# Kernel optimization log

Hardware: AMD Instinct MI355X
Metric: run time of the kernel (lower is better)

## Reference

```python
import math
import jax, jax.numpy as jnp
import numpy as np
from jax import lax

TAU_P = 0.5  # forward arg tau_p, fixed

def _grid_boxes(H, W, g):
    boxes = []
    for r in range(g):
        for c in range(g):
            x0 = int(round(c * (W / float(g)))); y0 = int(round(r * (H / float(g))))
            x1 = int(round((c + 1) * (W / float(g)))) - 1; y1 = int(round((r + 1) * (H / float(g)))) - 1
            boxes.append((x0, y0, x1, y1))
    return boxes

def _box_masks(H, W, g):
    bs = _grid_boxes(H, W, g)
    m = np.zeros((len(bs), H, W), np.float32)
    for i, (x0, y0, x1, y1) in enumerate(bs):
        m[i, y0:y1 + 1, x0:x1 + 1] = 1.0
    return jnp.asarray(m)

def _ln(x, g, b, eps=1e-5):
    mu = x.mean(-1, keepdims=True)
    v = jnp.var(x, axis=-1, keepdims=True)
    return (x - mu) * lax.rsqrt(v + eps) * g + b

def _l2n(x):
    return x / jnp.maximum(jnp.linalg.norm(x, axis=-1, keepdims=True), 1e-12)

def _forward(x, conv1_w, proj_w, proj_b, ln1_g, ln1_b, Wqkv, bqkv, Wo, bo,
             ln2_g, ln2_b, W1, b1, W2, b2, tln_g, tln_b, slot_q, cls_w, cls_b,
             use_spmask, spmask_grid):
    d = slot_q.shape[1]; M = slot_q.shape[0]; nhead = 4; dh = d // nhead
    # conv1 (1->150, k9 s2 p4) + exact gelu + 1x1 proj to d_model
    h = lax.conv_general_dilated(x, conv1_w, (2, 2), [(4, 4), (4, 4)],
                                 dimension_numbers=('NCHW', 'OIHW', 'NCHW'))
    h = jax.nn.gelu(h, approximate=False)
    h = jnp.einsum('bchw,dc->bdhw', h, proj_w) + proj_b[None, :, None, None]
    B, _, H, W = h.shape
    tokens = h.transpose(0, 2, 3, 1).reshape(B, H * W, d)  # (B,N,d)
    # pre-norm transformer encoder layer (1 layer)
    t1 = _ln(tokens, ln1_g, ln1_b)
    qkv = t1 @ Wqkv.T + bqkv
    q, k, v = jnp.split(qkv, 3, axis=-1)
    sh = lambda a: a.reshape(B, -1, nhead, dh).transpose(0, 2, 1, 3)
    q, k, v = sh(q), sh(k), sh(v)
    attn = jax.nn.softmax(jnp.einsum('bhnd,bhmd->bhnm', q, k) / math.sqrt(dh), axis=-1)
    o = jnp.einsum('bhnm,bhmd->bhnd', attn, v).transpose(0, 2, 1, 3).reshape(B, -1, d)
    tokens = tokens + o @ Wo.T + bo
    t2 = _ln(tokens, ln2_g, ln2_b)
    tokens = tokens + jax.nn.gelu(t2 @ W1.T + b1, approximate=False) @ W2.T + b2
    tokens = _ln(tokens, tln_g, tln_b)
    # slot attention logits, softmax over tokens
    A_logits = jnp.einsum('md,bnd->bmn', _l2n(slot_q), _l2n(tokens)) / math.sqrt(d)
    A_slot = jax.nn.softmax(A_logits, axis=2).reshape(B, M, H, W)
    if use_spmask:
        bm = _box_masks(H, W, spmask_grid)               # (G,H,W) static 0/1 masks
        mass = jnp.einsum('bmhw,ghw->bmg', A_slot, bm)   # per-cell mass
        _, top2 = lax.top_k(mass, 2)                     # (B,M,2) top-2 cells
        umask = jnp.maximum(bm[top2[..., 0]], bm[top2[..., 1]])  # union mask (B,M,H,W)
        A_eff = A_slot * umask
        s = jnp.maximum(A_eff.reshape(B, M, -1).sum(-1), 1e-8)
        A_eff = A_eff / s[:, :, None, None]
        m2 = A_eff.reshape(B, M, -1).sum(-1)             # post-renorm mass (torch order)
        z = (m2 - m2.mean(axis=1, keepdims=True)) / TAU_P
    else:
        A_eff = A_slot
        lse = jax.nn.logsumexp(A_logits, axis=2)
        z = (lse - lse.mean(axis=1, keepdims=True)) / TAU_P
    P = jax.nn.softmax(z, axis=1)                        # (B,M)
    S = jnp.einsum('bmn,bnd->bmd', A_eff.reshape(B, M, H * W), tokens)
    S = _l2n(S)
    slot_logits = S @ cls_w.T + cls_b                    # (B,M,C)
    return (slot_logits * P[..., None]).sum(axis=1)      # (B,C)

def setup_inputs() -> dict:
    key = jax.random.key(0)
    ks = jax.random.split(key, 16)
    d, M, C, dff = 64, 12, 47, 256
    n = lambda k, shape, s=0.05: (jax.random.normal(k, shape, dtype=jnp.float32) * s)
    return {
        'x': jax.random.normal(ks[0], (2048, 1, 28, 28), dtype=jnp.float32),
        'conv1_w': n(ks[1], (150, 1, 9, 9), 0.1),
        'proj_w': n(ks[2], (d, 150), 0.1), 'proj_b': jnp.zeros((d,), jnp.float32),
        'ln1_g': jnp.ones((d,), jnp.float32), 'ln1_b': jnp.zeros((d,), jnp.float32),
        'Wqkv': n(ks[3], (3 * d, d), 0.1), 'bqkv': jnp.zeros((3 * d,), jnp.float32),
        'Wo': n(ks[4], (d, d), 0.1), 'bo': jnp.zeros((d,), jnp.float32),
        'ln2_g': jnp.ones((d,), jnp.float32), 'ln2_b': jnp.zeros((d,), jnp.float32),
        'W1': n(ks[5], (dff, d), 0.1), 'b1': jnp.zeros((dff,), jnp.float32),
        'W2': n(ks[6], (d, dff), 0.1), 'b2': jnp.zeros((d,), jnp.float32),
        'tln_g': jnp.ones((d,), jnp.float32), 'tln_b': jnp.zeros((d,), jnp.float32),
        'slot_q': n(ks[7], (M, d), 1.0 / math.sqrt(d)),
        'cls_w': n(ks[8], (C, d), 0.1), 'cls_b': jnp.zeros((C,), jnp.float32),
        'use_spmask': 1, 'spmask_grid': 2,
    }

def reference(x, conv1_w, proj_w, proj_b, ln1_g, ln1_b, Wqkv, bqkv, Wo, bo,
              ln2_g, ln2_b, W1, b1, W2, b2, tln_g, tln_b, slot_q, cls_w, cls_b,
              use_spmask, spmask_grid):
    return _forward(x, conv1_w, proj_w, proj_b, ln1_g, ln1_b, Wqkv, bqkv, Wo, bo,
                    ln2_g, ln2_b, W1, b1, W2, b2, tln_g, tln_b, slot_q, cls_w, cls_b,
                    use_spmask, spmask_grid)
```

## Files before the change

### kernel.cpp

```cpp
#include <hip/hip_runtime.h>
#include <math.h>

typedef _Float16 half_t;
typedef __attribute__((ext_vector_type(2))) _Float16 half2t;
typedef __attribute__((ext_vector_type(4))) _Float16 half4;
typedef __attribute__((ext_vector_type(8))) _Float16 half8;
typedef __attribute__((ext_vector_type(4))) float f32x4;

__device__ __forceinline__ f32x4 MFMA16(half4 a, half4 b, f32x4 c) {
  return __builtin_amdgcn_mfma_f32_16x16x16f16(a, b, c, 0, 0, 0);
}
__device__ __forceinline__ f32x4 MFMA32(half8 a, half8 b, f32x4 c) {
  return __builtin_amdgcn_mfma_f32_16x16x32_f16(a, b, c, 0, 0, 0);
}

#if __has_builtin(__builtin_amdgcn_exp2f)
#define EXP2F(x) __builtin_amdgcn_exp2f(x)
#else
#define EXP2F(x) exp2f(x)
#endif

__device__ __forceinline__ half2t cvt_pk(float a, float b) {
#if __has_builtin(__builtin_amdgcn_cvt_pkrtz)
  return __builtin_bit_cast(half2t, __builtin_amdgcn_cvt_pkrtz(a, b));
#else
  half2t r; r[0] = (half_t)a; r[1] = (half_t)b; return r;
#endif
}
__device__ __forceinline__ half4 PK4(float a, float b, float c, float d) {
  half2t lo = cvt_pk(a, b), hi = cvt_pk(c, d);
  return __builtin_shufflevector(lo, hi, 0, 1, 2, 3);
}

__device__ __forceinline__ int SWi(int row, int col) {
  return (row << 6) | (((((col >> 2) ^ row) & 15)) << 2) | (col & 3);
}
__device__ __forceinline__ int SW4i(int row, int q) {
  return (row << 6) | ((((q ^ row) & 15)) << 2);
}
__device__ __forceinline__ int XH8W(int t, int k0) {
  return (t << 6) | ((((k0 >> 3) ^ t) & 7) << 3) | (k0 & 7);
}
__device__ __forceinline__ int XH8R(int t, int u8) {
  return (t << 6) | (((u8 ^ t) & 7) << 3);
}

__device__ __forceinline__ float fast_gelu(float v) {
  float x = 0.70710678118654752f * v;
  float ax = fabsf(x);
  float t = 1.0f / fmaf(0.3275911f, ax, 1.0f);
  float poly = t * fmaf(t, fmaf(t, fmaf(t, fmaf(t, 1.061405429f, -1.453152027f),
                                        1.421413741f), -0.284496736f), 0.254829592f);
  float e = EXP2F(-1.4426950408889634f * ax * ax);
  float erfax = fmaf(-poly, e, 1.0f);
  float er = __builtin_copysignf(erfax, x);
  return 0.5f * v * (1.0f + er);
}

__global__ void k_prepack(const float* __restrict__ conv_w,
                          const float* __restrict__ proj_w,
                          const float* __restrict__ Wqkv,
                          const float* __restrict__ Wo,
                          const float* __restrict__ W1,
                          const float* __restrict__ W2,
                          half_t* __restrict__ dst) {
  int id = blockIdx.x * 512 + threadIdx.x;
  if (id < 7552) {
    int unit = id >> 6, ln = id & 63;
    int li = ln & 15, g8 = (ln >> 4) * 8;
    float v[8];
    if (unit < 24) {
      int rt = unit >> 1, ks2 = unit & 1;
      const float* s = &Wqkv[(rt * 16 + li) * 64 + ks2 * 32 + g8];
#pragma unroll
      for (int r = 0; r < 8; ++r) v[r] = s[r];
    } else if (unit < 56) {
      int u = unit - 24, rt = u >> 1, ks2 = u & 1;
      const float* s = &W1[(rt * 16 + li) * 64 + ks2 * 32 + g8];
#pragma unroll
      for (int r = 0; r < 8; ++r) v[r] = s[r];
    } else if (unit < 88) {
      int u = unit - 56, ct = u >> 3, ks2 = u & 7;
      const float* s = &W2[(ct * 16 + li) * 256 + ks2 * 32 + g8];
#pragma unroll
      for (int r = 0; r < 8; ++r) v[r] = s[r];
    } else {
      int u = unit - 88, ct = u / 3, ks2 = u - ct * 3;
      int row = ct * 16 + li;
#pragma unroll
      for (int r = 0; r < 8; ++r) {
        int col = ks2 * 32 + g8 + r;
        v[r] = (row < 150 && col < 81) ? conv_w[row * 81 + col] : 0.f;
      }
    }
    half8 o;
#pragma unroll
    for (int r = 0; r < 8; ++r) o[r] = (half_t)v[r];
    ((half8*)dst)[id] = o;
  } else if (id < 11136) {
    int id2 = id - 7552;
    int unit = id2 >> 6, ln = id2 & 63;
    int li = ln & 15, gq = (ln >> 4) * 4;
    float v[4];
    if (unit < 16) {
      int ct = unit >> 2, h = unit & 3;
      const float* s = &Wo[(ct * 16 + li) * 64 + h * 16 + gq];
#pragma unroll
      for (int r = 0; r < 4; ++r) v[r] = s[r];
    } else {
      int u = unit - 16, dt = u / 10, ct = u - dt * 10;
#pragma unroll
      for (int r = 0; r < 4; ++r) {
        int col = ct * 16 + gq + r;
        v[r] = (col < 150) ? proj_w[(dt * 16 + li) * 150 + col] : 0.f;
      }
    }
    half4 o;
#pragma unroll
    for (int r = 0; r < 4; ++r) o[r] = (half_t)v[r];
    ((half4*)(dst + 60416))[id2] = o;
  }
}

__global__ __launch_bounds__(512, 4) void k_net(
    const float* __restrict__ x,
    const half8* __restrict__ WQ8, const half8* __restrict__ W18,
    const half8* __restrict__ W28, const half8* __restrict__ Wc8,
    const half4* __restrict__ WO4, const half4* __restrict__ Pw4,
    const float* __restrict__ proj_b,
    const float* __restrict__ ln1_g, const float* __restrict__ ln1_b,
    const float* __restrict__ bqkv, const float* __restrict__ bo,
    const float* __restrict__ ln2_g, const float* __restrict__ ln2_b,
    const float* __restrict__ b1, const float* __restrict__ b2,
    const float* __restrict__ tln_g, const float* __restrict__ tln_b,
    float* __restrict__ tokens) {
  extern __shared__ __align__(16) char pool[];
  half_t* xsh = (half_t*)pool;
  half_t* Xh = (half_t*)pool;
  half_t* Kb = (half_t*)(pool + 26624);
  half_t* VT = (half_t*)(pool + 43264);
  half8* W1S = (half8*)(pool + 26624);
  half8* W2S = (half8*)(pool + 34816);
  half_t* Hb = (half_t*)(pool + 43008);
  float* OS = (float*)pool;

  const int b = blockIdx.x, tid = threadIdx.x;
  const int wv = tid >> 6, ln = tid & 63, g = ln >> 4, li = ln & 15;
  const size_t base = (size_t)b * 12544;
  const half_t h1 = (half_t)1.f;
  const half4 ones = {h1, h1, h1, h1};

  f32x4 res[2][4];
#pragma unroll
  for (int qi = 0; qi < 2; ++qi)
#pragma unroll
    for (int ct = 0; ct < 4; ++ct) res[qi][ct] = f32x4{0.f, 0.f, 0.f, 0.f};

  for (int i = tid; i < 1260; i += 512) xsh[i] = (half_t)0.f;
  __syncthreads();
  for (int i = tid; i < 784; i += 512) {
    int r = i / 28, c = i - r * 28;
    xsh[(r + 4) * 36 + c + 4] = (half_t)x[b * 784 + i];
  }
  __syncthreads();

#pragma unroll
  for (int qi = 0; qi < 2; ++qi) {
    int qt = wv + 8 * qi;
    if (qt < 13) {
      int pp = qt * 16 + li;
      int pc = (pp < 196) ? pp : 195;
      int oy = pc / 14, ox = pc - oy * 14;
      int pbase = oy * 72 + ox * 2;
      half8 bf[3];
#pragma unroll
      for (int ks2 = 0; ks2 < 3; ++ks2) {
#pragma unroll
        for (int j = 0; j < 8; ++j) {
          int tap = ks2 * 32 + g * 8 + j;
          half_t v = (half_t)0.f;
          if (tap <= 80) {
            int ky = tap / 9;
            v = xsh[pbase + ky * 27 + tap];
          }
          bf[ks2][j] = v;
        }
      }
#pragma unroll
      for (int ct = 0; ct < 10; ++ct) {
        f32x4 acc = {0.f, 0.f, 0.f, 0.f};
#pragma unroll
        for (int ks2 = 0; ks2 < 3; ++ks2)
          acc = MFMA32(Wc8[(ct * 3 + ks2) * 64 + ln], bf[ks2], acc);
        half4 hf = PK4(fast_gelu(acc[0]), fast_gelu(acc[1]),
                       fast_gelu(acc[2]), fast_gelu(acc[3]));
#pragma unroll
        for (int dt = 0; dt < 4; ++dt)
          res[qi][dt] = MFMA16(Pw4[(dt * 10 + ct) * 64 + ln], hf, res[qi][dt]);
      }
#pragma unroll
      for (int dt = 0; dt < 4; ++dt) {
        float4 pb4 = *(const float4*)&proj_b[dt * 16 + g * 4];
        res[qi][dt][0] += pb4.x; res[qi][dt][1] += pb4.y;
        res[qi][dt][2] += pb4.z; res[qi][dt][3] += pb4.w;
      }
    }
  }
  __syncthreads();

  for (int i = tid; i < 768; i += 512)
    Xh[(196 + (i >> 6)) * 64 + (i & 63)] = (half_t)0.f;
#pragma unroll
  for (int qi = 0; qi < 2; ++qi) {
    int qt = wv + 8 * qi;
    if (qt < 13) {
      float sum = 0.f;
#pragma unroll
      for (int ct = 0; ct < 4; ++ct)
#pragma unroll
        for (int r = 0; r < 4; ++r) sum += res[qi][ct][r];
      sum += __shfl_xor(sum, 16, 64);
      sum += __shfl_xor(sum, 32, 64);
      float mu = sum * 0.015625f;
      float vs = 0.f;
#pragma unroll
      for (int ct = 0; ct < 4; ++ct)
#pragma unroll
        for (int r = 0; r < 4; ++r) { float d = res[qi][ct][r] - mu; vs += d * d; }
      vs += __shfl_xor(vs, 16, 64);
      vs += __shfl_xor(vs, 32, 64);
      float rs = rsqrtf(vs * 0.015625f + 1e-5f);
      int t = qt * 16 + li;
      if (t < 196) {
#pragma unroll
        for (int ct = 0; ct < 4; ++ct) {
          int k0 = ct * 16 + g * 4;
          float4 gg = *(const float4*)&ln1_g[k0];
          float4 bb = *(const float4*)&ln1_b[k0];
          *(half4*)&Xh[XH8W(t, k0)] =
              PK4((res[qi][ct][0] - mu) * rs * gg.x + bb.x,
                  (res[qi][ct][1] - mu) * rs * gg.y + bb.y,
                  (res[qi][ct][2] - mu) * rs * gg.z + bb.z,
                  (res[qi][ct][3] - mu) * rs * gg.w + bb.w);
        }
      }
    }
  }
  __syncthreads();

  half4 qf[2][4];
#pragma unroll
  for (int qi = 0; qi < 2; ++qi) {
    int qt = wv + 8 * qi;
    if (qt < 13) {
#pragma unroll
      for (int h = 0; h < 4; ++h) {
        f32x4 acc = {0.f, 0.f, 0.f, 0.f};
#pragma unroll
        for (int ks2 = 0; ks2 < 2; ++ks2)
          acc = MFMA32(WQ8[(h * 2 + ks2) * 64 + ln],
                       *(const half8*)&Xh[XH8R(qt * 16 + li, ks2 * 4 + g)], acc);
        const float SC = 0.36067376022224085f;
        qf[qi][h] = PK4((acc[0] + bqkv[h * 16 + g * 4 + 0]) * SC,
                        (acc[1] + bqkv[h * 16 + g * 4 + 1]) * SC,
                        (acc[2] + bqkv[h * 16 + g * 4 + 2]) * SC,
                        (acc[3] + bqkv[h * 16 + g * 4 + 3]) * SC);
      }
    }
  }

  for (int p = 0; p < 2; ++p) {
    {
      int rt4 = wv & 3, hh = rt4 & 1;
      bool isK = rt4 < 2;
      int rtg = (isK ? 4 : 8) + 2 * p + hh;
      half8 af[2];
#pragma unroll
      for (int ks2 = 0; ks2 < 2; ++ks2) af[ks2] = WQ8[(rtg * 2 + ks2) * 64 + ln];
      float bias[4];
      int brow = (isK ? 64 : 128) + (2 * p + hh) * 16 + g * 4;
#pragma unroll
      for (int r = 0; r < 4; ++r) bias[r] = bqkv[brow + r];
      int ta = (wv < 4) ? 0 : 7, tz = (wv < 4) ? 7 : 13;
      for (int tt = ta; tt < tz; ++tt) {
        int trow = tt * 16 + li;
        f32x4 acc = {0.f, 0.f, 0.f, 0.f};
#pragma unroll
        for (int ks2 = 0; ks2 < 2; ++ks2)
          acc = MFMA32(af[ks2], *(const half8*)&Xh[XH8R(trow, ks2 * 4 + g)], acc);
        if (isK) {
          *(half4*)&Kb[(hh * 208 + trow) * 20 + g * 4] =
              PK4(acc[0] + bias[0], acc[1] + bias[1],
                  acc[2] + bias[2], acc[3] + bias[3]);
        } else {
#pragma unroll
          for (int r = 0; r < 4; ++r)
            VT[(hh * 16 + g * 4 + r) * 212 + trow] = (half_t)(acc[r] + bias[r]);
        }
      }
    }
    __syncthreads();
#pragma unroll
    for (int qi = 0; qi < 2; ++qi) {
      int qt = wv + 8 * qi;
      if (qt < 13) {
#pragma unroll
        for (int hh = 0; hh < 2; ++hh) {
          int hglob = 2 * p + hh;
          f32x4 oa = {0.f, 0.f, 0.f, 0.f};
          f32x4 o1 = {0.f, 0.f, 0.f, 0.f};
#pragma unroll
          for (int nt = 0; nt < 13; ++nt) {
            f32x4 zz = {0.f, 0.f, 0.f, 0.f};
            f32x4 sv = MFMA16(*(const half4*)&Kb[(hh * 208 + nt * 16 + li) * 20 + g * 4],
                              qf[qi][hglob], zz);
            if (nt == 12 && g > 0) { sv[0] = -3e38f; sv[1] = -3e38f; sv[2] = -3e38f; sv[3] = -3e38f; }
            half4 pf = PK4(EXP2F(sv[0]), EXP2F(sv[1]), EXP2F(sv[2]), EXP2F(sv[3]));
            oa = MFMA16(*(const half4*)&VT[(hh * 16 + li) * 212 + nt * 16 + g * 4],
                        pf, oa);
            o1 = MFMA16(ones, pf, o1);
          }
          float inv = 1.0f / o1[0];
          half4 of = PK4(oa[0] * inv, oa[1] * inv, oa[2] * inv, oa[3] * inv);
#pragma unroll
          for (int ct = 0; ct < 4; ++ct)
            res[qi][ct] = MFMA16(WO4[(ct * 4 + hglob) * 64 + ln], of, res[qi][ct]);
        }
      }
    }
    __syncthreads();
  }
#pragma unroll
  for (int qi = 0; qi < 2; ++qi) {
    int qt = wv + 8 * qi;
    if (qt < 13) {
#pragma unroll
      for (int ct = 0; ct < 4; ++ct) {
        float4 bb = *(const float4*)&bo[ct * 16 + g * 4];
        res[qi][ct][0] += bb.x; res[qi][ct][1] += bb.y;
        res[qi][ct][2] += bb.z; res[qi][ct][3] += bb.w;
      }
    }
  }

#pragma unroll
  for (int qi = 0; qi < 2; ++qi) {
    int qt = wv + 8 * qi;
    if (qt < 13) {
      float sum = 0.f;
#pragma unroll
      for (int ct = 0; ct < 4; ++ct)
#pragma unroll
        for (int r = 0; r < 4; ++r) sum += res[qi][ct][r];
      sum += __shfl_xor(sum, 16, 64);
      sum += __shfl_xor(sum, 32, 64);
      float mu = sum * 0.015625f;
      float vs = 0.f;
#pragma unroll
      for (int ct = 0; ct < 4; ++ct)
#pragma unroll
        for (int r = 0; r < 4; ++r) { float d = res[qi][ct][r] - mu; vs += d * d; }
      vs += __shfl_xor(vs, 16, 64);
      vs += __shfl_xor(vs, 32, 64);
      float rs = rsqrtf(vs * 0.015625f + 1e-5f);
      int t = qt * 16 + li;
      if (t < 196) {
#pragma unroll
        for (int ct = 0; ct < 4; ++ct) {
          int k0 = ct * 16 + g * 4;
          float4 gg = *(const float4*)&ln2_g[k0];
          float4 bb = *(const float4*)&ln2_b[k0];
          *(half4*)&Xh[XH8W(t, k0)] =
              PK4((res[qi][ct][0] - mu) * rs * gg.x + bb.x,
                  (res[qi][ct][1] - mu) * rs * gg.y + bb.y,
                  (res[qi][ct][2] - mu) * rs * gg.z + bb.z,
                  (res[qi][ct][3] - mu) * rs * gg.w + bb.w);
        }
      }
    }
  }
  __syncthreads();

  for (int ch = 0; ch < 4; ++ch) {
    {
      int u = tid >> 6, l2 = tid & 63;
      int lnt = u >> 1, ks2 = u & 1;
      W1S[u * 64 + l2] = W18[((ch * 4 + lnt) * 2 + ks2) * 64 + l2];
      int ct = u >> 1, k2 = u & 1;
      W2S[u * 64 + l2] = W28[(ct * 8 + ch * 2 + k2) * 64 + l2];
    }
    __syncthreads();
#pragma unroll
    for (int j = 0; j < 7; ++j) {
      int u = wv + 8 * j;
      if (u < 52) {
        int mt = u >> 2, lnt = u & 3;
        f32x4 acc = {0.f, 0.f, 0.f, 0.f};
#pragma unroll
        for (int ks2 = 0; ks2 < 2; ++ks2)
          acc = MFMA32(*(const half8*)&Xh[XH8R(mt * 16 + li, ks2 * 4 + g)],
                       W1S[(lnt * 2 + ks2) * 64 + ln], acc);
        float bb = b1[ch * 64 + lnt * 16 + li];
#pragma unroll
        for (int r = 0; r < 4; ++r)
          Hb[XH8W(mt * 16 + g * 4 + r, lnt * 16 + li)] = (half_t)fast_gelu(acc[r] + bb);
      }
    }
    __syncthreads();
#pragma unroll
    for (int qi = 0; qi < 2; ++qi) {
      int qt = wv + 8 * qi;
      if (qt < 13) {
#pragma unroll
        for (int ct = 0; ct < 4; ++ct)
#pragma unroll
          for (int k2 = 0; k2 < 2; ++k2)
            res[qi][ct] = MFMA32(W2S[(ct * 2 + k2) * 64 + ln],
                                 *(const half8*)&Hb[XH8R(qt * 16 + li, k2 * 4 + g)],
                                 res[qi][ct]);
      }
    }
    __syncthreads();
  }
#pragma unroll
  for (int qi = 0; qi < 2; ++qi) {
    int qt = wv + 8 * qi;
    if (qt < 13) {
#pragma unroll
      for (int ct = 0; ct < 4; ++ct) {
        float4 bb = *(const float4*)&b2[ct * 16 + g * 4];
        res[qi][ct][0] += bb.x; res[qi][ct][1] += bb.y;
        res[qi][ct][2] += bb.z; res[qi][ct][3] += bb.w;
      }
    }
  }

#pragma unroll
  for (int qi = 0; qi < 2; ++qi) {
    int qt = wv + 8 * qi;
    if (qt < 13) {
      float sum = 0.f;
#pragma unroll
      for (int ct = 0; ct < 4; ++ct)
#pragma unroll
        for (int r = 0; r < 4; ++r) sum += res[qi][ct][r];
      sum += __shfl_xor(sum, 16, 64);
      sum += __shfl_xor(sum, 32, 64);
      float mu = sum * 0.015625f;
      float vs = 0.f;
#pragma unroll
      for (int ct = 0; ct < 4; ++ct)
#pragma unroll
        for (int r = 0; r < 4; ++r) { float d = res[qi][ct][r] - mu; vs += d * d; }
      vs += __shfl_xor(vs, 16, 64);
      vs += __shfl_xor(vs, 32, 64);
      float rs = rsqrtf(vs * 0.015625f + 1e-5f);
#pragma unroll
      for (int ct = 0; ct < 4; ++ct) {
        float4 gg = *(const float4*)&tln_g[ct * 16 + g * 4];
        float4 bb = *(const float4*)&tln_b[ct * 16 + g * 4];
        float4 o;
        o.x = (res[qi][ct][0] - mu) * rs * gg.x + bb.x;
        o.y = (res[qi][ct][1] - mu) * rs * gg.y + bb.y;
        o.z = (res[qi][ct][2] - mu) * rs * gg.z + bb.z;
        o.w = (res[qi][ct][3] - mu) * rs * gg.w + bb.w;
        *(float4*)&OS[wv * 1088 + li * 68 + ct * 16 + g * 4] = o;
      }
#pragma unroll
      for (int rep = 0; rep < 4; ++rep) {
        int r4 = rep * 64 + ln;
        int row = r4 >> 4, q = r4 & 15;
        int pp = qt * 16 + row;
        if (pp < 196)
          *(float4*)&tokens[base + (size_t)pp * 64 + q * 4] =
              *(const float4*)&OS[wv * 1088 + row * 68 + q * 4];
      }
    }
  }
}

__global__ __launch_bounds__(256) void k_slots(
    const float* __restrict__ tokens, const float* __restrict__ slot_q,
    const float* __restrict__ cls_w, const float* __restrict__ cls_b,
    const int* __restrict__ use_spmask_p, const int* __restrict__ grid_p,
    float* __restrict__ out) {
  __shared__ float TOK[12544];
  __shared__ float Abuf[12 * 196];
  __shared__ float SQS[12 * 64];
  __shared__ float INV[196];
  __shared__ float VV[64];
  __shared__ float Pv[12];
  __shared__ float M2[12];
  __shared__ float ISN[12];
  __shared__ float ZS[2];

  const int b = blockIdx.x, tid = threadIdx.x;
  const size_t base = (size_t)b * 12544;
  (void)grid_p;

  for (int i = tid; i < 12544; i += 256) {
    int t = i >> 6, c = i & 63;
    TOK[SWi(t, c)] = tokens[base + i];
  }
  __syncthreads();
  if (tid < 196) {
    float ss = 0.f;
#pragma unroll
    for (int q = 0; q < 16; ++q) {
      float4 v = *(const float4*)&TOK[SW4i(tid, q)];
      ss += v.x * v.x + v.y * v.y + v.z * v.z + v.w * v.w;
    }
    INV[tid] = 1.0f / fmaxf(sqrtf(ss), 1e-12f);
  }
  if (tid < 192) {
    int m = tid >> 4, l = tid & 15;
    float ss = 0.f;
#pragma unroll
    for (int c = l; c < 64; c += 16) {
      float v = slot_q[m * 64 + c];
      ss += v * v;
    }
#pragma unroll
    for (int mm = 8; mm; mm >>= 1) ss += __shfl_xor(ss, mm, 64);
    float invq = 1.0f / fmaxf(sqrtf(ss), 1e-12f);
#pragma unroll
    for (int c = l; c < 64; c += 16) SQS[m * 64 + c] = slot_q[m * 64 + c] * invq;
  }
  __syncthreads();
  for (int i = tid; i < 2352; i += 256) {
    int m = i / 196, n = i - m * 196;
    float d = 0.f;
#pragma unroll
    for (int q = 0; q < 16; ++q) {
      float4 tv = *(const float4*)&TOK[SW4i(n, q)];
      float4 sv = *(const float4*)&SQS[m * 64 + q * 4];
      d += tv.x * sv.x + tv.y * sv.y + tv.z * sv.z + tv.w * sv.w;
    }
    Abuf[i] = d * INV[n] * 0.125f;
  }
  __syncthreads();
  const int use_spmask = *use_spmask_p;
  if (tid < 192) {
    int m = tid >> 4, l = tid & 15;
    float* Am = Abuf + m * 196;
    float mx = -1e30f;
    for (int n = l; n < 196; n += 16) mx = fmaxf(mx, Am[n]);
#pragma unroll
    for (int mm = 8; mm; mm >>= 1) mx = fmaxf(mx, __shfl_xor(mx, mm, 64));
    float se = 0.f, mc0 = 0.f, mc1 = 0.f, mc2 = 0.f, mc3 = 0.f;
    for (int n = l; n < 196; n += 16) {
      float e = __expf(Am[n] - mx);
      Am[n] = e;
      se += e;
      int yy = n / 14, xx = n - yy * 14;
      int cell = ((yy >= 7) ? 2 : 0) + ((xx >= 7) ? 1 : 0);
      mc0 += (cell == 0) ? e : 0.f;
      mc1 += (cell == 1) ? e : 0.f;
      mc2 += (cell == 2) ? e : 0.f;
      mc3 += (cell == 3) ? e : 0.f;
    }
#pragma unroll
    for (int mm = 8; mm; mm >>= 1) {
      se += __shfl_xor(se, mm, 64);
      mc0 += __shfl_xor(mc0, mm, 64);
      mc1 += __shfl_xor(mc1, mm, 64);
      mc2 += __shfl_xor(mc2, mm, 64);
      mc3 += __shfl_xor(mc3, mm, 64);
    }
    float invse = 1.0f / se;
    if (use_spmask) {
      int g1 = 0; float bv1 = mc0;
      if (mc1 > bv1) { bv1 = mc1; g1 = 1; }
      if (mc2 > bv1) { bv1 = mc2; g1 = 2; }
      if (mc3 > bv1) { bv1 = mc3; g1 = 3; }
      int g2 = -1; float bv2 = -1e30f;
      if (g1 != 0 && mc0 > bv2) { bv2 = mc0; g2 = 0; }
      if (g1 != 1 && mc1 > bv2) { bv2 = mc1; g2 = 1; }
      if (g1 != 2 && mc2 > bv2) { bv2 = mc2; g2 = 2; }
      if (g1 != 3 && mc3 > bv2) { bv2 = mc3; g2 = 3; }
      float sacc = 0.f;
      for (int n = l; n < 196; n += 16) {
        float a = Am[n] * invse;
        Am[n] = a;
        int yy = n / 14, xx = n - yy * 14;
        int cell = ((yy >= 7) ? 2 : 0) + ((xx >= 7) ? 1 : 0);
        sacc += (cell == g1 || cell == g2) ? a : 0.f;
      }
#pragma unroll
      for (int mm = 8; mm; mm >>= 1) sacc += __shfl_xor(sacc, mm, 64);
      float invs = 1.0f / fmaxf(sacc, 1e-8f);
      float m2acc = 0.f;
      for (int n = l; n < 196; n += 16) {
        int yy = n / 14, xx = n - yy * 14;
        int cell = ((yy >= 7) ? 2 : 0) + ((xx >= 7) ? 1 : 0);
        float a = (cell == g1 || cell == g2) ? (Am[n] * invs) : 0.f;
        Am[n] = a;
        m2acc += a;
      }
#pragma unroll
      for (int mm = 8; mm; mm >>= 1) m2acc += __shfl_xor(m2acc, mm, 64);
      if (l == 0) M2[m] = m2acc;
    } else {
      for (int n = l; n < 196; n += 16) Am[n] *= invse;
      if (l == 0) M2[m] = mx + logf(se);
    }
  }
  __syncthreads();
  if (tid == 0) {
    float mean = 0.f;
    for (int m = 0; m < 12; ++m) mean += M2[m];
    mean *= (1.0f / 12.0f);
    float zmax = -1e30f;
    for (int m = 0; m < 12; ++m) {
      float z = (M2[m] - mean) * 2.0f;
      Pv[m] = z;
      zmax = fmaxf(zmax, z);
    }
    float seP = 0.f;
    for (int m = 0; m < 12; ++m) {
      float e = __expf(Pv[m] - zmax);
      Pv[m] = e;
      seP += e;
    }
    float invP = 1.0f / seP;
    float sump = 0.f;
    for (int m = 0; m < 12; ++m) {
      float p = Pv[m] * invP;
      Pv[m] = p;
      sump += p;
    }
    ZS[0] = sump;
  }
  __syncthreads();
  for (int i = tid; i < 768; i += 256) {
    int m = i >> 6, c = i & 63;
    float a2 = 0.f;
    const float* Am = Abuf + m * 196;
    for (int n = 0; n < 196; ++n) a2 += Am[n] * TOK[SWi(n, c)];
    SQS[m * 64 + c] = a2;
  }
  __syncthreads();
  if (tid < 192) {
    int m = tid >> 4, l = tid & 15;
    float ss = 0.f;
#pragma unroll
    for (int c = l; c < 64; c += 16) {
      float v = SQS[m * 64 + c];
      ss += v * v;
    }
#pragma unroll
    for (int mm = 8; mm; mm >>= 1) ss += __shfl_xor(ss, mm, 64);
    if (l == 0) ISN[m] = 1.0f / fmaxf(sqrtf(ss), 1e-12f);
  }
  __syncthreads();
  if (tid < 64) {
    float v = 0.f;
#pragma unroll
    for (int m = 0; m < 12; ++m) v += Pv[m] * ISN[m] * SQS[m * 64 + tid];
    VV[tid] = v;
  }
  __syncthreads();
  if (tid < 47) {
    float a2 = 0.f;
#pragma unroll
    for (int q = 0; q < 16; ++q) {
      float4 w = *(const float4*)&cls_w[tid * 64 + q * 4];
      float4 v = *(const float4*)&VV[q * 4];
      a2 += w.x * v.x + w.y * v.y + w.z * v.z + w.w * v.w;
    }
    out[(size_t)b * 47 + tid] = a2 + cls_b[tid] * ZS[0];
  }
}

extern "C" void kernel_launch(void* const* d_in, const int* in_sizes, int n_in,
                              void* d_out, int out_size, void* d_ws, size_t ws_size,
                              hipStream_t stream) {
  (void)n_in; (void)out_size; (void)ws_size;
  const float* x      = (const float*)d_in[0];
  const float* conv_w = (const float*)d_in[1];
  const float* proj_w = (const float*)d_in[2];
  const float* proj_b = (const float*)d_in[3];
  const float* ln1_g  = (const float*)d_in[4];
  const float* ln1_b  = (const float*)d_in[5];
  const float* Wqkv   = (const float*)d_in[6];
  const float* bqkv   = (const float*)d_in[7];
  const float* Wo     = (const float*)d_in[8];
  const float* bo     = (const float*)d_in[9];
  const float* ln2_g  = (const float*)d_in[10];
  const float* ln2_b  = (const float*)d_in[11];
  const float* W1     = (const float*)d_in[12];
  const float* b1     = (const float*)d_in[13];
  const float* W2     = (const float*)d_in[14];
  const float* b2     = (const float*)d_in[15];
  const float* tln_g  = (const float*)d_in[16];
  const float* tln_b  = (const float*)d_in[17];
  const float* slot_q = (const float*)d_in[18];
  const float* cls_w  = (const float*)d_in[19];
  const float* cls_b  = (const float*)d_in[20];
  const int* use_spm  = (const int*)d_in[21];
  const int* spgrid   = (const int*)d_in[22];

  const int B = in_sizes[0] / 784;
  half_t* wsh = (half_t*)d_ws;
  const half8* WQ8 = (const half8*)wsh;
  const half8* W18 = (const half8*)(wsh + 12288);
  const half8* W28 = (const half8*)(wsh + 28672);
  const half8* Wc8 = (const half8*)(wsh + 45056);
  const half4* WO4 = (const half4*)(wsh + 60416);
  const half4* Pw4 = (const half4*)(wsh + 64512);
  float* tokens = (float*)((char*)d_ws + 163840);

  k_prepack<<<22, 512, 0, stream>>>(conv_w, proj_w, Wqkv, Wo, W1, W2, wsh);

  const int shnet = 69632;
  (void)hipFuncSetAttribute((const void*)k_net,
                            hipFuncAttributeMaxDynamicSharedMemorySize, shnet);
  k_net<<<B, 512, shnet, stream>>>(x, WQ8, W18, W28, Wc8, WO4, Pw4, proj_b,
                                   ln1_g, ln1_b, bqkv, bo, ln2_g, ln2_b,
                                   b1, b2, tln_g, tln_b, tokens);

  k_slots<<<B, 256, 0, stream>>>(tokens, slot_q, cls_w, cls_b, use_spm, spgrid,
                                 (float*)d_out);
}
```

Baseline: 399.8 us.

## Fuse slot-attention kernel into transformer kernel, keeping tokens in LDS

```diff
diff --git a/kernel.cpp b/kernel.cpp
--- a/kernel.cpp
+++ b/kernel.cpp
@@ -133,7 +133,9 @@
     const float* __restrict__ ln2_g, const float* __restrict__ ln2_b,
     const float* __restrict__ b1, const float* __restrict__ b2,
     const float* __restrict__ tln_g, const float* __restrict__ tln_b,
-    float* __restrict__ tokens) {
+    const float* __restrict__ slot_q, const float* __restrict__ cls_w,
+    const float* __restrict__ cls_b, const int* __restrict__ use_spmask_p,
+    float* __restrict__ out) {
   extern __shared__ __align__(16) char pool[];
   half_t* xsh = (half_t*)pool;
   half_t* Xh = (half_t*)pool;
@@ -142,11 +144,18 @@
   half8* W1S = (half8*)(pool + 26624);
   half8* W2S = (half8*)(pool + 34816);
   half_t* Hb = (half_t*)(pool + 43008);
-  float* OS = (float*)pool;
+  float* TOK = (float*)pool;
+  float* Abuf = (float*)(pool + 50176);
+  float* SQS = (float*)(pool + 59584);
+  float* INV = (float*)(pool + 62656);
+  float* VV = (float*)(pool + 63440);
+  float* Pv = (float*)(pool + 63696);
+  float* M2 = (float*)(pool + 63744);
+  float* ISN = (float*)(pool + 63792);
+  float* ZS = (float*)(pool + 63840);
 
   const int b = blockIdx.x, tid = threadIdx.x;
   const int wv = tid >> 6, ln = tid & 63, g = ln >> 4, li = ln & 15;
-  const size_t base = (size_t)b * 12544;
   const half_t h1 = (half_t)1.f;
   const half4 ones = {h1, h1, h1, h1};
 
@@ -455,54 +464,25 @@
       vs += __shfl_xor(vs, 16, 64);
       vs += __shfl_xor(vs, 32, 64);
       float rs = rsqrtf(vs * 0.015625f + 1e-5f);
-#pragma unroll
-      for (int ct = 0; ct < 4; ++ct) {
-        float4 gg = *(const float4*)&tln_g[ct * 16 + g * 4];
-        float4 bb = *(const float4*)&tln_b[ct * 16 + g * 4];
-        float4 o;
-        o.x = (res[qi][ct][0] - mu) * rs * gg.x + bb.x;
-        o.y = (res[qi][ct][1] - mu) * rs * gg.y + bb.y;
-        o.z = (res[qi][ct][2] - mu) * rs * gg.z + bb.z;
-        o.w = (res[qi][ct][3] - mu) * rs * gg.w + bb.w;
-        *(float4*)&OS[wv * 1088 + li * 68 + ct * 16 + g * 4] = o;
-      }
-#pragma unroll
-      for (int rep = 0; rep < 4; ++rep) {
-        int r4 = rep * 64 + ln;
-        int row = r4 >> 4, q = r4 & 15;
-        int pp = qt * 16 + row;
-        if (pp < 196)
-          *(float4*)&tokens[base + (size_t)pp * 64 + q * 4] =
-              *(const float4*)&OS[wv * 1088 + row * 68 + q * 4];
-      }
-    }
-  }
-}
-
-__global__ __launch_bounds__(256) void k_slots(
-    const float* __restrict__ tokens, const float* __restrict__ slot_q,
-    const float* __restrict__ cls_w, const float* __restrict__ cls_b,
-    const int* __restrict__ use_spmask_p, const int* __restrict__ grid_p,
-    float* __restrict__ out) {
-  __shared__ float TOK[12544];
-  __shared__ float Abuf[12 * 196];
-  __shared__ float SQS[12 * 64];
-  __shared__ float INV[196];
-  __shared__ float VV[64];
-  __shared__ float Pv[12];
-  __shared__ float M2[12];
-  __shared__ float ISN[12];
-  __shared__ float ZS[2];
-
-  const int b = blockIdx.x, tid = threadIdx.x;
-  const size_t base = (size_t)b * 12544;
-  (void)grid_p;
-
-  for (int i = tid; i < 12544; i += 256) {
-    int t = i >> 6, c = i & 63;
-    TOK[SWi(t, c)] = tokens[base + i];
-  }
-  __syncthreads();
+      int t = qt * 16 + li;
+      if (t < 196) {
+#pragma unroll
+        for (int ct = 0; ct < 4; ++ct) {
+          int k0 = ct * 16 + g * 4;
+          float4 gg = *(const float4*)&tln_g[k0];
+          float4 bb = *(const float4*)&tln_b[k0];
+          float4 o;
+          o.x = (res[qi][ct][0] - mu) * rs * gg.x + bb.x;
+          o.y = (res[qi][ct][1] - mu) * rs * gg.y + bb.y;
+          o.z = (res[qi][ct][2] - mu) * rs * gg.z + bb.z;
+          o.w = (res[qi][ct][3] - mu) * rs * gg.w + bb.w;
+          *(float4*)&TOK[SWi(t, k0)] = o;
+        }
+      }
+    }
+  }
+  __syncthreads();
+
   if (tid < 196) {
     float ss = 0.f;
 #pragma unroll
@@ -527,7 +507,7 @@
     for (int c = l; c < 64; c += 16) SQS[m * 64 + c] = slot_q[m * 64 + c] * invq;
   }
   __syncthreads();
-  for (int i = tid; i < 2352; i += 256) {
+  for (int i = tid; i < 2352; i += 512) {
     int m = i / 196, n = i - m * 196;
     float d = 0.f;
 #pragma unroll
@@ -632,7 +612,7 @@
     ZS[0] = sump;
   }
   __syncthreads();
-  for (int i = tid; i < 768; i += 256) {
+  for (int i = tid; i < 768; i += 512) {
     int m = i >> 6, c = i & 63;
     float a2 = 0.f;
     const float* Am = Abuf + m * 196;
@@ -698,7 +678,6 @@
   const float* cls_w  = (const float*)d_in[19];
   const float* cls_b  = (const float*)d_in[20];
   const int* use_spm  = (const int*)d_in[21];
-  const int* spgrid   = (const int*)d_in[22];
 
   const int B = in_sizes[0] / 784;
   half_t* wsh = (half_t*)d_ws;
@@ -708,7 +687,6 @@
   const half8* Wc8 = (const half8*)(wsh + 45056);
   const half4* WO4 = (const half4*)(wsh + 60416);
   const half4* Pw4 = (const half4*)(wsh + 64512);
-  float* tokens = (float*)((char*)d_ws + 163840);
 
   k_prepack<<<22, 512, 0, stream>>>(conv_w, proj_w, Wqkv, Wo, W1, W2, wsh);
 
@@ -717,8 +695,6 @@
                             hipFuncAttributeMaxDynamicSharedMemorySize, shnet);
   k_net<<<B, 512, shnet, stream>>>(x, WQ8, W18, W28, Wc8, WO4, Pw4, proj_b,
                                    ln1_g, ln1_b, bqkv, bo, ln2_g, ln2_b,
-                                   b1, b2, tln_g, tln_b, tokens);
-
-  k_slots<<<B, 256, 0, stream>>>(tokens, slot_q, cls_w, cls_b, use_spm, spgrid,
-                                 (float*)d_out);
-}
+                                   b1, b2, tln_g, tln_b, slot_q, cls_w, cls_b,
+                                   use_spm, (float*)d_out);
+}
```

After: 364.4 us. 1.1x faster.
